# Kernel tuning notes

Hardware: AMD Instinct MI355X
Metric: run time of the kernel (lower is better)

The kernel has to match this reference:

```python
import math
import jax, jax.numpy as jnp
import numpy as np

C = 64
GRID = 2

def _conv1x1(x, W, b):
    # 1x1 conv == channel-mixing matmul: [B,C,H,W] x [O,C] -> [B,O,H,W]
    return jnp.einsum('bchw,oc->bohw', x, W) + b[None, :, None, None]

def setup_inputs() -> dict:
    key = jax.random.key(0)
    ks = jax.random.split(key, 11)
    s = 1.0 / math.sqrt(C)
    def w(k):
        return jax.random.normal(k, (C, C), dtype=jnp.float32) * s
    def bias(k):
        return jax.random.normal(k, (C,), dtype=jnp.float32) * 0.02
    return {
        'x': jax.random.normal(ks[0], (2, C, 128, 128), dtype=jnp.float32),
        'Wq': w(ks[1]), 'bq': bias(ks[2]),
        'Wk': w(ks[3]), 'bk': bias(ks[4]),
        'Wa': w(ks[5]), 'ba': bias(ks[6]),
        'Wb': w(ks[7]), 'bb': bias(ks[8]),
        'Wo': w(ks[9]), 'bo': bias(ks[10]),
    }

def reference(x, Wq, bq, Wk, bk, Wa, ba, Wb, bb, Wo, bo):
    B, c, H, W = x.shape
    g = GRID
    rh, rw = H // g, W // g  # H,W chosen divisible by grid -> no reflect pad
    N = rh * rw
    R = g * g

    q = _conv1x1(x, Wq, bq)
    k = _conv1x1(x, Wk, bk)
    a = _conv1x1(x, Wa, ba)
    bt = _conv1x1(x, Wb, bb)

    def regionize(t):
        # [B,C,H,W] -> [B, R, C, N] with N = rh*rw row-major per region
        return t.reshape(B, c, g, rh, g, rw).transpose(0, 2, 4, 1, 3, 5).reshape(B, R, c, N)

    qr, kr, ar, br = regionize(q), regionize(k), regionize(a), regionize(bt)

    # attn[b,r,n,m] = softmax_m( q^T k / sqrt(C) )
    attn = jax.nn.softmax(jnp.einsum('brcn,brcm->brnm', qr, kr) / math.sqrt(c), axis=-1)

    # out_r = alpha @ attn + beta @ attn^T
    out = (jnp.einsum('brcj,brjm->brcm', ar, attn)
           + jnp.einsum('brcj,brmj->brcm', br, attn))

    # [B,R,C,N] -> [B,C,H,W]
    out = out.reshape(B, g, g, c, rh, rw).transpose(0, 3, 1, 4, 2, 5).reshape(B, c, H, W)
    return _conv1x1(out, Wo, bo)
```

## Files before the change

kernel.cpp:

```cpp
#include <hip/hip_runtime.h>


typedef __attribute__((ext_vector_type(8)))  short bf16x8;
typedef __attribute__((ext_vector_type(16))) float f32x16;

#define MFMA32(a, b, c) __builtin_amdgcn_mfma_f32_32x32x16_bf16(a, b, c, 0, 0, 0)

constexpr int REG_ELEMS = 4096 * 64;
constexpr size_t QP_OFF  = 0;
constexpr size_t KP_OFF  = 4u  << 20;
constexpr size_t ATL_OFF = 8u  << 20;
constexpr size_t BTL_OFF = 12u << 20;
constexpr size_t OUTP_OFF= 16u << 20;
constexpr size_t LNV_OFF = 20u << 20;

constexpr float QSCALE = 0.18033688011112042f;

__device__ __forceinline__ short f2bf(float f) {
    union { float f; unsigned u; } v; v.f = f;
    unsigned r = v.u + 0x7fffu + ((v.u >> 16) & 1u);
    return (short)(r >> 16);
}
__device__ __forceinline__ float bf2f(short s) {
    union { unsigned u; float f; } v; v.u = ((unsigned)(unsigned short)s) << 16;
    return v.f;
}
__device__ __forceinline__ unsigned fbits(float f) {
    union { float f; unsigned u; } v; v.f = f; return v.u;
}
__device__ __forceinline__ unsigned pack_trunc(float e0, float e1) {
    return __builtin_amdgcn_perm(fbits(e1), fbits(e0), 0x07060302u);
}
__device__ __forceinline__ f32x16 zero16() {
    f32x16 z;
    #pragma unroll
    for (int i = 0; i < 16; ++i) z[i] = 0.f;
    return z;
}
__device__ __forceinline__ float fexp2(float x) {
#if __has_builtin(__builtin_amdgcn_exp2f)
    return __builtin_amdgcn_exp2f(x);
#else
    return exp2f(x);
#endif
}
__device__ __forceinline__ void permswap32(unsigned& a, unsigned& b, bool hi) {
#if __has_builtin(__builtin_amdgcn_permlane32_swap)
    auto r = __builtin_amdgcn_permlane32_swap(a, b, false, false);
    a = r[0]; b = r[1];
#elif __has_builtin(__builtin_amdgcn_permlane32_swap_b32)
    auto r = __builtin_amdgcn_permlane32_swap_b32(a, b, false, false);
    a = r[0]; b = r[1];
#else
    unsigned ax = (unsigned)__shfl_xor((int)a, 32);
    unsigned bx = (unsigned)__shfl_xor((int)b, 32);
    unsigned na = hi ? bx : a;
    unsigned nb = hi ? b  : ax;
    a = na; b = nb;
#endif
}

typedef __attribute__((address_space(1))) const unsigned char as1_t;
typedef __attribute__((address_space(3))) unsigned char as3_t;
__device__ __forceinline__ void stage16(const void* g, void* l) {
    __builtin_amdgcn_global_load_lds((as1_t*)g, (as3_t*)l, 16, 0, 0);
}

__global__ __launch_bounds__(256) void k_conv_in(
    const float* __restrict__ x,
    const float* __restrict__ Wq, const float* __restrict__ bq,
    const float* __restrict__ Wk, const float* __restrict__ bk,
    const float* __restrict__ Wa, const float* __restrict__ ba,
    const float* __restrict__ Wb, const float* __restrict__ bb,
    char* __restrict__ ws)
{
    const int tid  = threadIdx.x;
    const int blk  = blockIdx.x;
    const int wseg = blk & 1;
    const int h    = (blk >> 1) & 127;
    const int b    = blk >> 8;
    const int br   = b * 4 + (h >> 6) * 2 + wseg;
    const int n0   = (h & 63) * 64;

    __shared__ float xs[64][68];
    __shared__ short trans[2][64][72];

    const float* xp = x + ((size_t)b * 64 * 16384) + (size_t)h * 128 + wseg * 64;
    #pragma unroll
    for (int r = 0; r < 4; ++r) {
        int idx = r * 256 + tid;
        int c   = idx >> 4;
        int w4  = (idx & 15) << 2;
        *(float4*)&xs[c][w4] = *(const float4*)(xp + (size_t)c * 16384 + w4);
    }
    __syncthreads();

    const int mat = tid >> 6;
    const int oc  = tid & 63;
    const float* Wsel = (mat == 0) ? Wq : (mat == 1) ? Wk : (mat == 2) ? Wa : Wb;
    const float* bsel = (mat == 0) ? bq : (mat == 1) ? bk : (mat == 2) ? ba : bb;

    float acc[64];
    const float bias = bsel[oc];
    #pragma unroll
    for (int w = 0; w < 64; ++w) acc[w] = bias;

    #pragma unroll 8
    for (int c = 0; c < 64; ++c) {
        const float wv = Wsel[oc * 64 + c];
        #pragma unroll
        for (int w = 0; w < 64; ++w) acc[w] = fmaf(wv, xs[c][w], acc[w]);
    }

    if (mat == 0) {
        #pragma unroll
        for (int w = 0; w < 64; ++w) acc[w] *= QSCALE;
    }

    if (mat >= 2) {
        short tmp[64];
        #pragma unroll
        for (int w = 0; w < 64; ++w) tmp[w] = f2bf(acc[w]);
        short* base = (short*)(ws + (mat == 2 ? ATL_OFF : BTL_OFF))
                      + (size_t)br * REG_ELEMS;
        const int sw = (oc >> 1) & 3;
        #pragma unroll
        for (int w8 = 0; w8 < 8; ++w8) {
            int tile = (n0 >> 5) + (w8 >> 2);
            int segp = (w8 & 3) ^ sw;
            *(uint4*)(base + (size_t)tile * 2048 + oc * 32 + segp * 8) =
                *(uint4*)&tmp[w8 * 8];
        }
    } else {
        #pragma unroll
        for (int w = 0; w < 64; ++w) trans[mat][w][oc] = f2bf(acc[w]);
    }
    __syncthreads();

    #pragma unroll
    for (int rep = 0; rep < 4; ++rep) {
        int idx  = rep * 256 + tid;
        int mat2 = idx >> 9;
        int row  = (idx >> 3) & 63;
        int seg  = idx & 7;
        short* dst = (short*)(ws + (mat2 ? KP_OFF : QP_OFF))
                     + (size_t)br * REG_ELEMS + (size_t)(n0 + row) * 64
                     + (seg ^ (row & 7)) * 8;
        *(uint4*)dst = *(uint4*)&trans[mat2][row][seg * 8];
    }
}

__global__ __launch_bounds__(256, 2) void k_stats(char* __restrict__ ws)
{
    const int tid  = threadIdx.x;
    const int br   = blockIdx.x & 7;
    const int nt   = blockIdx.x >> 3;
    const int lane = tid & 63;
    const int w    = tid >> 6;
    const int wn   = w & 1;
    const int wi   = w >> 1;
    const int col  = lane & 31;
    const int l5   = lane >> 5;

    const short* Qb  = (const short*)(ws + QP_OFF) + (size_t)br * REG_ELEMS;
    const char*  Kbb = ws + KP_OFF + (size_t)br * REG_ELEMS * 2;

    __shared__ __align__(16) char smem[17408];

    const int nrow = nt * 64 + wn * 32 + col;
    bf16x8 afr[4];
    #pragma unroll
    for (int s = 0; s < 4; ++s)
        afr[s] = *(const bf16x8*)(Qb + (size_t)nrow * 64 + (((2*s+l5) ^ (col & 7)) * 8));

    float sm[16];
    #pragma unroll
    for (int r = 0; r < 16; ++r) sm[r] = 0.f;

    {
        const char* g = Kbb + (size_t)w * 2048 + lane * 16;
        char* l = smem + w * 2048;
        stage16(g, l); stage16(g + 1024, l + 1024);
    }

    #pragma unroll 2
    for (int slab = 0; slab < 64; ++slab) {
        __syncthreads();
        if (slab + 1 < 64) {
            const char* g = Kbb + (size_t)(slab + 1) * 8192 + w * 2048 + lane * 16;
            char* l = smem + ((slab + 1) & 1) * 8192 + w * 2048;
            stage16(g, l); stage16(g + 1024, l + 1024);
        }
        const short* Ks = (const short*)(smem + (slab & 1) * 8192);
        f32x16 d = zero16();
        #pragma unroll
        for (int s = 0; s < 4; ++s) {
            bf16x8 bf = *(const bf16x8*)(Ks + (wi * 32 + col) * 64
                                         + ((2*s+l5) ^ (col & 7)) * 8);
            d = MFMA32(afr[s], bf, d);
        }
        #pragma unroll
        for (int r = 0; r < 16; ++r) sm[r] += fexp2(d[r]);
    }

    #pragma unroll
    for (int off = 1; off < 32; off <<= 1)
        #pragma unroll
        for (int r = 0; r < 16; ++r) sm[r] += __shfl_xor(sm[r], off);

    __syncthreads();
    float* Lred = (float*)(smem + 16384);
    float* Larr = (float*)(smem + 16896);
    if (col == 0) {
        #pragma unroll
        for (int r = 0; r < 16; ++r)
            Lred[w * 32 + ((r & 3) + 8 * (r >> 2) + 4 * l5)] = sm[r];
    }
    __syncthreads();
    if (tid < 64) {
        int wn2 = tid >> 5, nl = tid & 31;
        float L = Lred[wn2 * 32 + nl] + Lred[(wn2 + 2) * 32 + nl];
        float li = 1.0f / L;
        Larr[tid] = li;
        ((float*)(ws + LNV_OFF))[(size_t)br * 4096 + nt * 64 + tid] = li;
    }
    __syncthreads();

    short* Ab = (short*)(ws + ATL_OFF) + (size_t)br * REG_ELEMS + (size_t)nt * 4096;
    #pragma unroll
    for (int rep = 0; rep < 2; ++rep) {
        int id = rep * 256 + tid;
        int t = id >> 8, c = (id >> 2) & 63, s = id & 3;
        int sg = s ^ ((c >> 1) & 3);
        int jl = t * 32 + sg * 8;
        short* p = Ab + (size_t)t * 2048 + c * 32 + s * 8;
        uint4 v = *(uint4*)p;
        short* sp = (short*)&v;
        short o[8];
        #pragma unroll
        for (int e = 0; e < 8; ++e) o[e] = f2bf(bf2f(sp[e]) * Larr[jl + e]);
        *(uint4*)p = *(uint4*)o;
    }
}

__global__ __launch_bounds__(256, 2) void k_attn(char* __restrict__ ws)
{
    const int tid  = threadIdx.x;
    const int br   = blockIdx.x & 7;
    const int mt   = blockIdx.x >> 3;
    const int lane = tid & 63;
    const int w    = tid >> 6;
    const int wm   = w & 1;
    const int wj   = w >> 1;
    const int col  = lane & 31;
    const int l5   = lane >> 5;
    const bool hi  = (l5 != 0);

    const char* Qbb = ws + QP_OFF  + (size_t)br * REG_ELEMS * 2;
    const char* Kbb = ws + KP_OFF  + (size_t)br * REG_ELEMS * 2;
    const char* Abb = ws + ATL_OFF + (size_t)br * REG_ELEMS * 2;
    const char* Bbb = ws + BTL_OFF + (size_t)br * REG_ELEMS * 2;
    const float* Lnv = (const float*)(ws + LNV_OFF) + (size_t)br * 4096;
    short* OutPb    = (short*)(ws + OUTP_OFF) + (size_t)br * REG_ELEMS;

    __shared__ __align__(16) char smem[32768];

    const int mrow = mt * 64 + wm * 32 + col;
    const short* msrc = (const short*)(wj == 0 ? Kbb : Qbb) + (size_t)mrow * 64;
    bf16x8 mf[4];
    #pragma unroll
    for (int s = 0; s < 4; ++s)
        mf[s] = *(const bf16x8*)(msrc + ((2*s+l5) ^ (col & 7)) * 8);

    f32x16 accL = zero16(), accH = zero16();

    const char* gsb = (w == 0) ? Qbb : (w == 1) ? Kbb : (w == 2) ? Abb : Bbb;

    {
        const char* g = gsb + lane * 16;
        char* l = smem + w * 4096 + lane * 16;
        #pragma unroll
        for (int i = 0; i < 4; ++i) stage16(g + i * 1024, l + i * 1024);
    }

    #pragma unroll 2
    for (int slab = 0; slab < 128; ++slab) {
        __syncthreads();
        if (slab + 1 < 128) {
            const char* g = gsb + (size_t)(slab + 1) * 4096 + lane * 16;
            char* l = smem + ((slab + 1) & 1) * 16384 + w * 4096 + lane * 16;
            #pragma unroll
            for (int i = 0; i < 4; ++i) stage16(g + i * 1024, l + i * 1024);
        }
        const char* sb = smem + (slab & 1) * 16384;
        const short* js = (const short*)(sb + (wj == 0 ? 0 : 4096));
        const short* ts = (const short*)(sb + (wj == 0 ? 8192 : 12288));

        f32x16 d = zero16();
        #pragma unroll
        for (int s = 0; s < 4; ++s) {
            bf16x8 a = *(const bf16x8*)(js + col * 64 + ((2*s+l5) ^ (col & 7)) * 8);
            d = MFMA32(a, mf[s], d);
        }

        unsigned Wp[8];
        #pragma unroll
        for (int q = 0; q < 4; ++q) {
            Wp[2*q]   = pack_trunc(fexp2(d[4*q]),   fexp2(d[4*q+1]));
            Wp[2*q+1] = pack_trunc(fexp2(d[4*q+2]), fexp2(d[4*q+3]));
        }

        #pragma unroll
        for (int k16 = 0; k16 < 2; ++k16) {
            unsigned u0 = Wp[4*k16+0], u1 = Wp[4*k16+1];
            unsigned u2 = Wp[4*k16+2], u3 = Wp[4*k16+3];
            permswap32(u0, u2, hi);
            permswap32(u1, u3, hi);
            union { uint4 u; bf16x8 v; } fr;
            fr.u.x = u0; fr.u.y = u1; fr.u.z = u2; fr.u.w = u3;

            const int swz = ((2*k16 + l5) ^ ((col >> 1) & 3)) * 8;
            bf16x8 bL = *(const bf16x8*)(ts + col * 32 + swz);
            bf16x8 bH = *(const bf16x8*)(ts + (col + 32) * 32 + swz);
            accL = MFMA32(fr.v, bL, accL);
            accH = MFMA32(fr.v, bH, accH);
        }
    }

    __syncthreads();
    float* red = (float*)smem;
    if (wj == 0) {
        #pragma unroll
        for (int r = 0; r < 16; ++r) {
            int ml = wm * 32 + (r & 3) + 8 * (r >> 2) + 4 * l5;
            red[ml * 68 + col]      = accL[r];
            red[ml * 68 + 32 + col] = accH[r];
        }
    }
    __syncthreads();
    if (wj == 1) {
        #pragma unroll
        for (int r = 0; r < 16; ++r) {
            int ml = wm * 32 + (r & 3) + 8 * (r >> 2) + 4 * l5;
            float li = Lnv[mt * 64 + ml];
            red[ml * 68 + col]      += li * accL[r];
            red[ml * 68 + 32 + col] += li * accH[r];
        }
    }
    __syncthreads();
    {
        const int m  = tid >> 2;
        const int c0 = (tid & 3) * 16;
        const float* rp = red + m * 68 + c0;
        uint4 p0, p1;
        p0.x = pack_trunc(rp[0],  rp[1]);  p0.y = pack_trunc(rp[2],  rp[3]);
        p0.z = pack_trunc(rp[4],  rp[5]);  p0.w = pack_trunc(rp[6],  rp[7]);
        p1.x = pack_trunc(rp[8],  rp[9]);  p1.y = pack_trunc(rp[10], rp[11]);
        p1.z = pack_trunc(rp[12], rp[13]); p1.w = pack_trunc(rp[14], rp[15]);
        short* orow = OutPb + (size_t)(mt * 64 + m) * 64 + c0;
        *(uint4*)orow       = p0;
        *(uint4*)(orow + 8) = p1;
    }
}

__global__ __launch_bounds__(64) void k_conv_out(
    const char* __restrict__ ws,
    const float* __restrict__ Wo, const float* __restrict__ bo,
    float* __restrict__ out)
{
    const int lane = threadIdx.x;
    const int br   = blockIdx.x & 7;
    const int nt   = blockIdx.x >> 3;
    const int col  = lane & 31;
    const int l5   = lane >> 5;

    const short* OutPb = (const short*)(ws + OUTP_OFF) + (size_t)br * REG_ELEMS;

    bf16x8 afr[4];
    const short* arow = OutPb + (size_t)(nt * 32 + col) * 64 + l5 * 8;
    #pragma unroll
    for (int s = 0; s < 4; ++s) afr[s] = *(const bf16x8*)(arow + s * 16);

    bf16x8 bw[2][4];
    #pragma unroll
    for (int oh = 0; oh < 2; ++oh) {
        const float* wrow = Wo + (size_t)(oh * 32 + col) * 64 + l5 * 8;
        #pragma unroll
        for (int s = 0; s < 4; ++s) {
            float4 f0 = *(const float4*)(wrow + s * 16);
            float4 f1 = *(const float4*)(wrow + s * 16 + 4);
            union { bf16x8 v; short sh[8]; } u;
            u.sh[0] = f2bf(f0.x); u.sh[1] = f2bf(f0.y);
            u.sh[2] = f2bf(f0.z); u.sh[3] = f2bf(f0.w);
            u.sh[4] = f2bf(f1.x); u.sh[5] = f2bf(f1.y);
            u.sh[6] = f2bf(f1.z); u.sh[7] = f2bf(f1.w);
            bw[oh][s] = u.v;
        }
    }

    f32x16 d0 = zero16(), d1 = zero16();
    #pragma unroll
    for (int s = 0; s < 4; ++s) {
        d0 = MFMA32(afr[s], bw[0][s], d0);
        d1 = MFMA32(afr[s], bw[1][s], d1);
    }

    const int b  = br >> 2;
    const int gi = (br >> 1) & 1;
    const int gj = br & 1;

    #pragma unroll
    for (int oh = 0; oh < 2; ++oh) {
        const int oc = oh * 32 + col;
        const float bias = bo[oc];
        const f32x16& d = oh ? d1 : d0;
        #pragma unroll
        for (int q = 0; q < 4; ++q) {
            int nloc = 8 * q + 4 * l5;
            int nreg = nt * 32 + nloc;
            int wp   = nreg & 63;
            int ip   = nreg >> 6;
            float4 v = make_float4(d[4*q+0] + bias, d[4*q+1] + bias,
                                   d[4*q+2] + bias, d[4*q+3] + bias);
            float* op = out + ((size_t)(b * 64 + oc)) * 16384
                        + (size_t)(gi * 64 + ip) * 128 + gj * 64 + wp;
            *(float4*)op = v;
        }
    }
}

extern "C" void kernel_launch(void* const* d_in, const int* in_sizes, int n_in,
                              void* d_out, int out_size, void* d_ws, size_t ws_size,
                              hipStream_t stream)
{
    const float* x  = (const float*)d_in[0];
    const float* Wq = (const float*)d_in[1];
    const float* bq = (const float*)d_in[2];
    const float* Wk = (const float*)d_in[3];
    const float* bk = (const float*)d_in[4];
    const float* Wa = (const float*)d_in[5];
    const float* ba = (const float*)d_in[6];
    const float* Wb = (const float*)d_in[7];
    const float* bb = (const float*)d_in[8];
    const float* Wo = (const float*)d_in[9];
    const float* bo = (const float*)d_in[10];
    char* ws   = (char*)d_ws;
    float* out = (float*)d_out;

    hipLaunchKernelGGL(k_conv_in,  dim3(512),  dim3(256), 0, stream,
                       x, Wq, bq, Wk, bk, Wa, ba, Wb, bb, ws);
    hipLaunchKernelGGL(k_stats,    dim3(512),  dim3(256), 0, stream, ws);
    hipLaunchKernelGGL(k_attn,     dim3(512),  dim3(256), 0, stream, ws);
    hipLaunchKernelGGL(k_conv_out, dim3(1024), dim3(64),  0, stream,
                       ws, Wo, bo, out);
}
```

Measured before the change: 232.0 us.

## Compute QKAB projection with split-bf16 MFMA instead of scalar FMA

Replaces the per-thread scalar fp32 FMA loop for the four 1x1 projections with 32x32x16 bf16 MFMA instructions. Inputs and weights are split into hi/lo bf16 parts and three MFMAs per k-step recover near-fp32 accuracy. Each wave now computes a 32x32 tile for all four matrices, loading weights directly into registers and writing through the same swizzled layouts. The aim is to cut the heavy VALU cost of the projection, at the price of extra conversion work and a small precision change.

```diff
diff --git a/kernel.cpp b/kernel.cpp
--- a/kernel.cpp
+++ b/kernel.cpp
@@ -95,45 +95,82 @@
     }
     __syncthreads();
 
-    const int mat = tid >> 6;
-    const int oc  = tid & 63;
-    const float* Wsel = (mat == 0) ? Wq : (mat == 1) ? Wk : (mat == 2) ? Wa : Wb;
-    const float* bsel = (mat == 0) ? bq : (mat == 1) ? bk : (mat == 2) ? ba : bb;
-
-    float acc[64];
-    const float bias = bsel[oc];
-    #pragma unroll
-    for (int w = 0; w < 64; ++w) acc[w] = bias;
-
-    #pragma unroll 8
-    for (int c = 0; c < 64; ++c) {
-        const float wv = Wsel[oc * 64 + c];
-        #pragma unroll
-        for (int w = 0; w < 64; ++w) acc[w] = fmaf(wv, xs[c][w], acc[w]);
-    }
-
-    if (mat == 0) {
-        #pragma unroll
-        for (int w = 0; w < 64; ++w) acc[w] *= QSCALE;
-    }
-
-    if (mat >= 2) {
-        short tmp[64];
-        #pragma unroll
-        for (int w = 0; w < 64; ++w) tmp[w] = f2bf(acc[w]);
-        short* base = (short*)(ws + (mat == 2 ? ATL_OFF : BTL_OFF))
-                      + (size_t)br * REG_ELEMS;
-        const int sw = (oc >> 1) & 3;
-        #pragma unroll
-        for (int w8 = 0; w8 < 8; ++w8) {
-            int tile = (n0 >> 5) + (w8 >> 2);
-            int segp = (w8 & 3) ^ sw;
-            *(uint4*)(base + (size_t)tile * 2048 + oc * 32 + segp * 8) =
-                *(uint4*)&tmp[w8 * 8];
-        }
-    } else {
-        #pragma unroll
-        for (int w = 0; w < 64; ++w) trans[mat][w][oc] = f2bf(acc[w]);
+    const int lane = tid & 63;
+    const int wid  = tid >> 6;
+    const int col  = lane & 31;
+    const int l5   = lane >> 5;
+    const int pH   = wid & 1;
+    const int oH   = wid >> 1;
+    const int px   = pH * 32 + col;
+    const int oc   = oH * 32 + col;
+
+    bf16x8 xhi[4], xlo[4];
+    #pragma unroll
+    for (int s = 0; s < 4; ++s) {
+        union { bf16x8 v; short sh[8]; } uh, ul;
+        #pragma unroll
+        for (int e = 0; e < 8; ++e) {
+            float xv = xs[s * 16 + l5 * 8 + e][px];
+            short hh = f2bf(xv);
+            uh.sh[e] = hh;
+            ul.sh[e] = f2bf(xv - bf2f(hh));
+        }
+        xhi[s] = uh.v; xlo[s] = ul.v;
+    }
+
+    #pragma unroll
+    for (int mat = 0; mat < 4; ++mat) {
+        const float* Wsel = (mat == 0) ? Wq : (mat == 1) ? Wk : (mat == 2) ? Wa : Wb;
+        const float* bsel = (mat == 0) ? bq : (mat == 1) ? bk : (mat == 2) ? ba : bb;
+
+        bf16x8 whi[4], wlo[4];
+        const float* wrow = Wsel + (size_t)oc * 64;
+        #pragma unroll
+        for (int s = 0; s < 4; ++s) {
+            float4 f0 = *(const float4*)(wrow + s * 16 + l5 * 8);
+            float4 f1 = *(const float4*)(wrow + s * 16 + l5 * 8 + 4);
+            float wf[8] = { f0.x, f0.y, f0.z, f0.w, f1.x, f1.y, f1.z, f1.w };
+            union { bf16x8 v; short sh[8]; } uh, ul;
+            #pragma unroll
+            for (int e = 0; e < 8; ++e) {
+                short hh = f2bf(wf[e]);
+                uh.sh[e] = hh;
+                ul.sh[e] = f2bf(wf[e] - bf2f(hh));
+            }
+            whi[s] = uh.v; wlo[s] = ul.v;
+        }
+
+        f32x16 d = zero16();
+        #pragma unroll
+        for (int s = 0; s < 4; ++s) {
+            d = MFMA32(xhi[s], whi[s], d);
+            d = MFMA32(xhi[s], wlo[s], d);
+            d = MFMA32(xlo[s], whi[s], d);
+        }
+
+        const float bias = bsel[oc];
+        if (mat < 2) {
+            const float sc = (mat == 0) ? QSCALE : 1.0f;
+            #pragma unroll
+            for (int r = 0; r < 16; ++r) {
+                int pxl = pH * 32 + (r & 3) + 8 * (r >> 2) + 4 * l5;
+                trans[mat][pxl][oc] = f2bf((d[r] + bias) * sc);
+            }
+        } else {
+            short* base = (short*)(ws + (mat == 2 ? ATL_OFF : BTL_OFF))
+                          + (size_t)br * REG_ELEMS;
+            const int sw   = (oc >> 1) & 3;
+            const int tile = (n0 >> 5) + pH;
+            #pragma unroll
+            for (int q = 0; q < 4; ++q) {
+                short tmp4[4];
+                #pragma unroll
+                for (int rr = 0; rr < 4; ++rr) tmp4[rr] = f2bf(d[4 * q + rr] + bias);
+                int segp = q ^ sw;
+                short* p = base + (size_t)tile * 2048 + oc * 32 + segp * 8 + 4 * l5;
+                *(uint2*)p = *(uint2*)tmp4;
+            }
+        }
     }
     __syncthreads();
 
```

New measurement: 206.1 us. 11.1% less time.
